# Kernel tuning notes

Hardware: AMD Instinct MI355X
Metric: run time of the kernel (lower is better)

## Reference

```python
import jax, jax.numpy as jnp
import numpy as np

N_NODES = 50000
N_EDGES = 600000
IN_CH, HID1, HID2, OUT_CH = 128, 256, 128, 2


def setup_inputs() -> dict:
    key = jax.random.key(0)
    ks = jax.random.split(key, 8)
    x = jax.random.normal(ks[0], (N_NODES, IN_CH), dtype=jnp.float32)
    edge_index = jax.random.randint(ks[1], (2, N_EDGES), 0, N_NODES, dtype=jnp.int64)
    # Glorot-style init for GCN linear weights
    def glorot(k, fan_in, fan_out):
        s = jnp.sqrt(6.0 / (fan_in + fan_out)).astype(jnp.float32)
        return jax.random.uniform(k, (fan_in, fan_out), jnp.float32, -s, s)
    return {
        "x": x,
        "W1": glorot(ks[2], IN_CH, HID1), "b1": jnp.zeros((HID1,), jnp.float32),
        "W2": glorot(ks[3], HID1, HID2), "b2": jnp.zeros((HID2,), jnp.float32),
        "W3": glorot(ks[4], HID2, OUT_CH), "b3": jnp.zeros((OUT_CH,), jnp.float32),
        "edge_index": edge_index,
    }


def _gcn_graph(edge_index, n_nodes):
    # Add self-loops (GCNConv default) and compute symmetric normalization
    loop = jnp.arange(n_nodes, dtype=edge_index.dtype)
    src = jnp.concatenate([edge_index[0], loop])
    dst = jnp.concatenate([edge_index[1], loop])
    ones = jnp.ones(src.shape[0], dtype=jnp.float32)
    deg = jax.ops.segment_sum(ones, dst, num_segments=n_nodes)
    dinv = jnp.where(deg > 0, jax.lax.rsqrt(deg), 0.0)
    norm = dinv[src] * dinv[dst]  # [E + N]
    return src, dst, norm


def _gcn_layer(h, W, b, src, dst, norm, n_nodes):
    h = h @ W                                   # [N, d_out]
    msg = h[src] * norm[:, None]                # gather + scale  [E+N, d_out]
    agg = jax.ops.segment_sum(msg, dst, num_segments=n_nodes)
    return agg + b


def reference(x, W1, b1, W2, b2, W3, b3, edge_index):
    n = x.shape[0]
    src, dst, norm = _gcn_graph(edge_index, n)
    h = jax.nn.relu(_gcn_layer(x, W1, b1, src, dst, norm, n))
    # dropout p=0.5 is identity in eval mode (training=False)
    h = jax.nn.relu(_gcn_layer(h, W2, b2, src, dst, norm, n))
    h = _gcn_layer(h, W3, b3, src, dst, norm, n)
    return jax.nn.log_softmax(h, axis=1)
```

## Files before the change

kernel.cpp:

```cpp
#include <hip/hip_runtime.h>
#include <hip/hip_bf16.h>
#include <math.h>

#define N_NODES 50000
#define N_EDGES 600000
#define E_TOT   (N_EDGES + N_NODES)
#define M_PAD   50048
#define NODE_STRIDE 32
#define DUMMY_ROWS 65536
#define CSR_CAP (N_NODES * NODE_STRIDE + 2048)

typedef __attribute__((ext_vector_type(8))) short bf16x8;
typedef __attribute__((ext_vector_type(4))) float f32x4;
typedef __attribute__((ext_vector_type(2))) float f32x2;
typedef __attribute__((ext_vector_type(8))) unsigned short u16x8;


__device__ __forceinline__ unsigned short f2bf(float f) {
    unsigned int u = __float_as_uint(f);
    unsigned int r = (u + 0x7fffu + ((u >> 16) & 1u)) >> 16;
    return (unsigned short)r;
}

__device__ __forceinline__ void acc_row(f32x2* acc, uint4 v) {
    acc[0] += (f32x2){__uint_as_float(v.x << 16), __uint_as_float(v.x & 0xffff0000u)};
    acc[1] += (f32x2){__uint_as_float(v.y << 16), __uint_as_float(v.y & 0xffff0000u)};
    acc[2] += (f32x2){__uint_as_float(v.z << 16), __uint_as_float(v.z & 0xffff0000u)};
    acc[3] += (f32x2){__uint_as_float(v.w << 16), __uint_as_float(v.w & 0xffff0000u)};
}

#define GLD_LDS16(g, l) __builtin_amdgcn_global_load_lds( \
    (__attribute__((address_space(1))) void*)(void*)(g), \
    (__attribute__((address_space(3))) void*)(l), 16, 0, 0)


__global__ void prep_kernel(const int* __restrict__ ei, int* __restrict__ cnt,
                            const float* __restrict__ W1, const float* __restrict__ W2,
                            unsigned short* __restrict__ W1t, unsigned short* __restrict__ W2t,
                            unsigned short* __restrict__ csr, unsigned short* __restrict__ xs,
                            unsigned short* __restrict__ t2b, float2* __restrict__ Ts) {
    const int NB_S = (E_TOT + 255) / 256;
    int b = blockIdx.x;
    if (b < NB_S) {
        int e = b * 256 + threadIdx.x;
        if (e >= E_TOT) return;
        int s, d;
        if (e < N_EDGES) { s = ei[e]; d = ei[N_EDGES + e]; }
        else             { s = d = e - N_EDGES; }
        int slot = atomicAdd(&cnt[d], 1);
        if (slot < NODE_STRIDE)
            csr[d * NODE_STRIDE + slot] = (unsigned short)s;
    } else if (b < NB_S + 128) {
        int i = (b - NB_S) * 256 + threadIdx.x;
        int k = i >> 8, n = i & 255;
        W1t[(size_t)n * 128 + k] = f2bf(W1[i]);
    } else if (b < NB_S + 256) {
        int i = (b - NB_S - 128) * 256 + threadIdx.x;
        int k = i >> 7, n = i & 127;
        W2t[(size_t)n * 256 + k] = f2bf(W2[i]);
    } else {
        int t = threadIdx.x;
        if (t < 16)
            *(uint4*)(xs + (size_t)(DUMMY_ROWS - 1) * 128 + t * 8) = make_uint4(0, 0, 0, 0);
        else if (t < 32)
            *(uint4*)(t2b + (size_t)(DUMMY_ROWS - 1) * 128 + (t - 16) * 8) = make_uint4(0, 0, 0, 0);
        else if (t == 32)
            Ts[DUMMY_ROWS - 1] = make_float2(0.f, 0.f);
    }
}


__global__ void scale_kernel(const int* __restrict__ cnt, const float* __restrict__ x,
                             unsigned short* __restrict__ xs, float* __restrict__ dinv) {
    const int NB_C = (N_NODES * 32 + 255) / 256;
    int b = blockIdx.x;
    if (b < NB_C) {
        int i = b * 256 + threadIdx.x;
        if (i >= N_NODES * 32) return;
        float d = rsqrtf((float)cnt[i >> 5]);
        float4 v = *(const float4*)(x + (size_t)i * 4);
        ushort4 o;
        o.x = f2bf(v.x * d); o.y = f2bf(v.y * d); o.z = f2bf(v.z * d); o.w = f2bf(v.w * d);
        *(ushort4*)(xs + (size_t)i * 4) = o;
    } else {
        int i = (b - NB_C) * 256 + threadIdx.x;
        if (i < N_NODES) dinv[i] = rsqrtf((float)cnt[i]);
    }
}


template<bool LAYER2>
__global__ __launch_bounds__(256) void agg_kernel(
    const unsigned short* __restrict__ Hs, const float* __restrict__ dinv,
    const int* __restrict__ cnt, const unsigned short* __restrict__ csr,
    const float* __restrict__ bias, const float* __restrict__ W3,
    unsigned short* __restrict__ outb, float2* __restrict__ Ts) {
    int wave = threadIdx.x >> 6;
    int lane = threadIdx.x & 63;
    int n = blockIdx.x * 4 + wave;
    if (n >= N_NODES) return;
    int quarter = lane >> 4;
    int q = lane & 15;
    f32x2 acc2[4] = {};
    int p0 = n * NODE_STRIDE;
    int pdeg = (cnt[n] + 15) & ~15;
    if (pdeg > NODE_STRIDE) pdeg = NODE_STRIDE;
    int pend = p0 + pdeg;
    int p = p0 + quarter * 4;
    ushort4 s4 = *(const ushort4*)(csr + p);
    while (p < pend) {
        int pn = p + 16;
        ushort4 n4 = *(const ushort4*)(csr + pn);
        uint4 v0 = *(const uint4*)(Hs + (size_t)s4.x * 128 + q * 8);
        uint4 v1 = *(const uint4*)(Hs + (size_t)s4.y * 128 + q * 8);
        uint4 v2 = *(const uint4*)(Hs + (size_t)s4.z * 128 + q * 8);
        uint4 v3 = *(const uint4*)(Hs + (size_t)s4.w * 128 + q * 8);
        acc_row(acc2, v0);
        acc_row(acc2, v1);
        acc_row(acc2, v2);
        acc_row(acc2, v3);
        p = pn; s4 = n4;
    }
    float* acc = (float*)acc2;
    #pragma unroll
    for (int i = 0; i < 8; ++i) {
        acc[i] += __shfl_xor(acc[i], 16);
        acc[i] += __shfl_xor(acc[i], 32);
    }
    float dn = dinv[n];
    if (!LAYER2) {
        if (quarter == 0) {
            u16x8 ov;
            #pragma unroll
            for (int i = 0; i < 8; ++i) ov[i] = f2bf(acc[i] * dn);
            *(u16x8*)(outb + (size_t)n * 128 + q * 8) = ov;
        }
    } else {
        float t0 = 0.f, t1 = 0.f;
        #pragma unroll
        for (int i = 0; i < 8; ++i) {
            int c = q * 8 + i;
            float h = fmaxf(acc[i] * dn + bias[c], 0.f);
            float2 w = ((const float2*)W3)[c];
            t0 += h * w.x; t1 += h * w.y;
        }
        #pragma unroll
        for (int off = 1; off < 16; off <<= 1) {
            t0 += __shfl_xor(t0, off);
            t1 += __shfl_xor(t1, off);
        }
        if (lane == 0) Ts[n] = make_float2(t0 * dn, t1 * dn);
    }
}


__global__ __launch_bounds__(256) void gemm12_kernel(
    const unsigned short* __restrict__ A,
    const unsigned short* __restrict__ W1t,
    const unsigned short* __restrict__ W2t,
    const float* __restrict__ b1,
    const float* __restrict__ rowscale,
    unsigned short* __restrict__ C,
    int M) {
    __shared__ __align__(16) unsigned short h1buf[128 * 256];
    __shared__ __align__(16) unsigned short Bs[64 * 128];
    int tid = threadIdx.x;
    int wave = tid >> 6, lane = tid & 63;
    int m0 = blockIdx.x * 128;
    int mm = lane & 15, kg = lane >> 4;
    int row0 = kg * 4;

    bf16x8 aPre[4][2];
    #pragma unroll
    for (int kt = 0; kt < 4; ++kt)
        #pragma unroll
        for (int i = 0; i < 2; ++i) {
            int m = wave * 32 + i * 16 + mm;
            aPre[kt][i] = *(const bf16x8*)(A + (size_t)(m0 + m) * 128 + kt * 32 + kg * 8);
        }

    int bb[4];
    #pragma unroll
    for (int j = 0; j < 4; ++j) bb[j] = (j * 16 + mm) * 128;
    int h1rd[2];
    #pragma unroll
    for (int i = 0; i < 2; ++i) h1rd[i] = (wave * 32 + i * 16 + mm) * 256;

    #pragma unroll 1
    for (int nt = 0; nt < 4; ++nt) {
        int n0 = nt * 64;
        #pragma unroll
        for (int it = 0; it < 4; ++it) {
            int ci = it * 256 + tid;
            int r = ci >> 4, c8 = (ci & 15) ^ (r & 15);
            const unsigned short* g = W1t + (size_t)(n0 + r) * 128 + c8 * 8;
            unsigned short* l = Bs + (size_t)(it * 256 + (tid & 192)) * 8;
            GLD_LDS16(g, l);
        }
        __syncthreads();
        f32x4 acc[2][4];
        #pragma unroll
        for (int i = 0; i < 2; ++i)
            #pragma unroll
            for (int j = 0; j < 4; ++j)
                acc[i][j] = (f32x4){0.f, 0.f, 0.f, 0.f};
        #pragma unroll
        for (int kt = 0; kt < 4; ++kt) {
            bf16x8 bfr[4];
            #pragma unroll
            for (int j = 0; j < 4; ++j)
                bfr[j] = *(const bf16x8*)(Bs + bb[j] + (((kt * 4 + kg) ^ mm) * 8));
            #pragma unroll
            for (int i = 0; i < 2; ++i)
                #pragma unroll
                for (int j = 0; j < 4; ++j)
                    acc[i][j] = __builtin_amdgcn_mfma_f32_16x16x32_bf16(aPre[kt][i], bfr[j], acc[i][j], 0, 0, 0);
        }
        float bj[4];
        #pragma unroll
        for (int j = 0; j < 4; ++j) bj[j] = b1[n0 + j * 16 + mm];
        #pragma unroll
        for (int i = 0; i < 2; ++i) {
            #pragma unroll
            for (int r = 0; r < 4; ++r) {
                int ml = wave * 32 + i * 16 + row0 + r;
                int rb = ml * 256, rx = ml & 15;
                #pragma unroll
                for (int j = 0; j < 4; ++j) {
                    int c = n0 + j * 16 + mm;
                    int c8 = c >> 3;
                    float v = fmaxf(acc[i][j][r] + bj[j], 0.f);
                    h1buf[rb + ((c8 ^ rx) * 8) + (c & 7)] = f2bf(v);
                }
            }
        }
        __syncthreads();
    }

    #pragma unroll 1
    for (int nh = 0; nh < 2; ++nh) {
        int n0 = nh * 64;
        f32x4 acc[2][4];
        #pragma unroll
        for (int i = 0; i < 2; ++i)
            #pragma unroll
            for (int j = 0; j < 4; ++j)
                acc[i][j] = (f32x4){0.f, 0.f, 0.f, 0.f};
        #pragma unroll 1
        for (int kh = 0; kh < 2; ++kh) {
            #pragma unroll
            for (int it = 0; it < 4; ++it) {
                int ci = it * 256 + tid;
                int r = ci >> 4, c8 = (ci & 15) ^ (r & 15);
                const unsigned short* g = W2t + (size_t)(n0 + r) * 256 + kh * 128 + c8 * 8;
                unsigned short* l = Bs + (size_t)(it * 256 + (tid & 192)) * 8;
                GLD_LDS16(g, l);
            }
            __syncthreads();
            #pragma unroll
            for (int kt = 0; kt < 4; ++kt) {
                bf16x8 af[2], bfr[4];
                int c8h = kh * 16 + kt * 4 + kg;
                #pragma unroll
                for (int i = 0; i < 2; ++i)
                    af[i] = *(const bf16x8*)(h1buf + h1rd[i] + ((c8h ^ mm) * 8));
                #pragma unroll
                for (int j = 0; j < 4; ++j)
                    bfr[j] = *(const bf16x8*)(Bs + bb[j] + (((kt * 4 + kg) ^ mm) * 8));
                #pragma unroll
                for (int i = 0; i < 2; ++i)
                    #pragma unroll
                    for (int j = 0; j < 4; ++j)
                        acc[i][j] = __builtin_amdgcn_mfma_f32_16x16x32_bf16(af[i], bfr[j], acc[i][j], 0, 0, 0);
            }
            __syncthreads();
        }
        #pragma unroll
        for (int i = 0; i < 2; ++i) {
            #pragma unroll
            for (int r = 0; r < 4; ++r) {
                int gm = m0 + wave * 32 + i * 16 + row0 + r;
                float sc = (gm < M) ? rowscale[gm] : 0.f;
                #pragma unroll
                for (int j = 0; j < 4; ++j) {
                    int gn = n0 + j * 16 + mm;
                    C[(size_t)gm * 128 + gn] = f2bf(acc[i][j][r] * sc);
                }
            }
        }
    }
}


__global__ void lsm_kernel(const float2* __restrict__ Ts, const float* __restrict__ dinv,
                           const int* __restrict__ cnt, const unsigned short* __restrict__ csr,
                           const float* __restrict__ b3, float* __restrict__ out) {
    int n = blockIdx.x * 256 + threadIdx.x;
    if (n >= N_NODES) return;
    float a0 = 0.f, a1 = 0.f;
    int p0 = n * NODE_STRIDE;
    int pdeg = (cnt[n] + 3) & ~3;
    if (pdeg > NODE_STRIDE) pdeg = NODE_STRIDE;
    int pend = p0 + pdeg;
    ushort4 s4 = *(const ushort4*)(csr + p0);
    for (int p = p0; p < pend; p += 4) {
        ushort4 n4 = *(const ushort4*)(csr + p + 4);
        float2 u0 = Ts[s4.x], u1 = Ts[s4.y], u2 = Ts[s4.z], u3 = Ts[s4.w];
        a0 += (u0.x + u1.x) + (u2.x + u3.x);
        a1 += (u0.y + u1.y) + (u2.y + u3.y);
        s4 = n4;
    }
    float dn = dinv[n];
    float v0 = a0 * dn + b3[0];
    float v1 = a1 * dn + b3[1];
    float m = fmaxf(v0, v1);
    float lse = m + logf(expf(v0 - m) + expf(v1 - m));
    out[n * 2 + 0] = v0 - lse;
    out[n * 2 + 1] = v1 - lse;
}


extern "C" void kernel_launch(void* const* d_in, const int* in_sizes, int n_in,
                              void* d_out, int out_size, void* d_ws, size_t ws_size,
                              hipStream_t stream) {
    const float* x  = (const float*)d_in[0];
    const float* W1 = (const float*)d_in[1];
    const float* b1 = (const float*)d_in[2];
    const float* W2 = (const float*)d_in[3];
    const float* b2 = (const float*)d_in[4];
    const float* W3 = (const float*)d_in[5];
    const float* b3 = (const float*)d_in[6];
    const int*   ei = (const int*)d_in[7];
    float* out = (float*)d_out;

    char* ws = (char*)d_ws;
    size_t off = 0;
    auto alloc = [&](size_t bytes) -> char* {
        char* p = ws + off;
        off = (off + bytes + 255) & ~(size_t)255;
        return p;
    };
    int*   cnt  = (int*)alloc(N_NODES * 4);
    float* dinv = (float*)alloc(N_NODES * 4);
    unsigned short* csr = (unsigned short*)alloc((size_t)CSR_CAP * 2);
    unsigned short* xs     = (unsigned short*)alloc((size_t)DUMMY_ROWS * 128 * 2);
    unsigned short* W1t    = (unsigned short*)alloc((size_t)256 * 128 * 2);
    unsigned short* W2t    = (unsigned short*)alloc((size_t)128 * 256 * 2);
    unsigned short* aggx_b = (unsigned short*)alloc((size_t)M_PAD * 128 * 2);
    unsigned short* t2b    = (unsigned short*)alloc((size_t)DUMMY_ROWS * 128 * 2);
    float2* Ts = (float2*)alloc((size_t)DUMMY_ROWS * 8);

    hipMemsetAsync(cnt, 0, N_NODES * 4, stream);
    hipMemsetAsync(csr, 0xFF, (size_t)CSR_CAP * 2, stream);

    const int NB_S = (E_TOT + 255) / 256;
    prep_kernel<<<NB_S + 256 + 1, 256, 0, stream>>>(
        ei, cnt, W1, W2, W1t, W2t, csr, xs, t2b, Ts);

    const int NB_C = (N_NODES * 32 + 255) / 256;
    const int NB_D = (N_NODES + 255) / 256;
    scale_kernel<<<NB_C + NB_D, 256, 0, stream>>>(cnt, x, xs, dinv);

    agg_kernel<false><<<(N_NODES + 3) / 4, 256, 0, stream>>>(
        xs, dinv, cnt, csr, nullptr, nullptr, aggx_b, nullptr);
    gemm12_kernel<<<M_PAD / 128, 256, 0, stream>>>(
        aggx_b, W1t, W2t, b1, dinv, t2b, N_NODES);
    agg_kernel<true><<<(N_NODES + 3) / 4, 256, 0, stream>>>(
        t2b, dinv, cnt, csr, b2, W3, nullptr, Ts);

    lsm_kernel<<<(N_NODES + 255) / 256, 256, 0, stream>>>(Ts, dinv, cnt, csr, b3, out);
}
```

Before: 199.4 us.

## Fuse layer-1 aggregation into the GEMM kernel and use 16-lane-per-node gather

The first neighbour aggregation now runs inside the fused GEMM kernel, so each 128-row block gathers its A tile straight into shared memory. This removes the aggregated-feature buffer and one kernel launch. The layer-2 aggregation now gives each node 16 lanes instead of a full wave, which avoids the cross-quarter shuffles and pads the degree to 4 instead of 16. The risk is that the gather inside the GEMM runs on only 391 blocks, one per 128 rows. Each thread group also walks 8 nodes one after another, which could expose gather latency and leave the GPU underused.

```diff
diff --git a/kernel.cpp b/kernel.cpp
--- a/kernel.cpp
+++ b/kernel.cpp
@@ -89,28 +89,207 @@
 }
 
 
-template<bool LAYER2>
-__global__ __launch_bounds__(256) void agg_kernel(
-    const unsigned short* __restrict__ Hs, const float* __restrict__ dinv,
+__global__ __launch_bounds__(256) void gemm12_kernel(
+    const unsigned short* __restrict__ Hs,
+    const float* __restrict__ dinv,
+    const int* __restrict__ cnt,
+    const unsigned short* __restrict__ csr,
+    const unsigned short* __restrict__ W1t,
+    const unsigned short* __restrict__ W2t,
+    const float* __restrict__ b1,
+    unsigned short* __restrict__ C,
+    int M) {
+    __shared__ __align__(16) unsigned short smem[128 * 256 + 64 * 128];
+    unsigned short* Atile = smem;
+    unsigned short* h1buf = smem;
+    unsigned short* Bs    = smem + 128 * 256;
+    int tid = threadIdx.x;
+    int wave = tid >> 6, lane = tid & 63;
+    int m0 = blockIdx.x * 128;
+    int mm = lane & 15, kg = lane >> 4;
+    int row0 = kg * 4;
+
+    {
+        int q = tid & 15;
+        int g = tid >> 4;
+        #pragma unroll 1
+        for (int nn = 0; nn < 8; ++nn) {
+            int r = g * 8 + nn;
+            int n = m0 + r;
+            f32x2 acc2[4] = {};
+            float dn = 0.f;
+            if (n < M) {
+                dn = dinv[n];
+                int p = n * NODE_STRIDE;
+                int pd = (cnt[n] + 3) & ~3;
+                if (pd > NODE_STRIDE) pd = NODE_STRIDE;
+                int pe = p + pd;
+                ushort4 s4 = *(const ushort4*)(csr + p);
+                while (p < pe) {
+                    int pn = p + 4;
+                    ushort4 nx = *(const ushort4*)(csr + pn);
+                    uint4 v0 = *(const uint4*)(Hs + (size_t)s4.x * 128 + q * 8);
+                    uint4 v1 = *(const uint4*)(Hs + (size_t)s4.y * 128 + q * 8);
+                    uint4 v2 = *(const uint4*)(Hs + (size_t)s4.z * 128 + q * 8);
+                    uint4 v3 = *(const uint4*)(Hs + (size_t)s4.w * 128 + q * 8);
+                    acc_row(acc2, v0);
+                    acc_row(acc2, v1);
+                    acc_row(acc2, v2);
+                    acc_row(acc2, v3);
+                    p = pn; s4 = nx;
+                }
+            }
+            float* acc = (float*)acc2;
+            u16x8 ov;
+            #pragma unroll
+            for (int i2 = 0; i2 < 8; ++i2) ov[i2] = f2bf(acc[i2] * dn);
+            *(u16x8*)(Atile + r * 128 + ((q ^ (r & 15)) * 8)) = ov;
+        }
+    }
+    __syncthreads();
+
+    bf16x8 aPre[4][2];
+    #pragma unroll
+    for (int kt = 0; kt < 4; ++kt)
+        #pragma unroll
+        for (int i = 0; i < 2; ++i) {
+            int m = wave * 32 + i * 16 + mm;
+            aPre[kt][i] = *(const bf16x8*)(Atile + m * 128 + (((kt * 4 + kg) ^ (m & 15)) * 8));
+        }
+
+    int bb[4];
+    #pragma unroll
+    for (int j = 0; j < 4; ++j) bb[j] = (j * 16 + mm) * 128;
+    int h1rd[2];
+    #pragma unroll
+    for (int i = 0; i < 2; ++i) h1rd[i] = (wave * 32 + i * 16 + mm) * 256;
+
+    #pragma unroll 1
+    for (int nt = 0; nt < 4; ++nt) {
+        int n0 = nt * 64;
+        #pragma unroll
+        for (int it = 0; it < 4; ++it) {
+            int ci = it * 256 + tid;
+            int r = ci >> 4, c8 = (ci & 15) ^ (r & 15);
+            const unsigned short* g = W1t + (size_t)(n0 + r) * 128 + c8 * 8;
+            unsigned short* l = Bs + (size_t)(it * 256 + (tid & 192)) * 8;
+            GLD_LDS16(g, l);
+        }
+        __syncthreads();
+        f32x4 acc[2][4];
+        #pragma unroll
+        for (int i = 0; i < 2; ++i)
+            #pragma unroll
+            for (int j = 0; j < 4; ++j)
+                acc[i][j] = (f32x4){0.f, 0.f, 0.f, 0.f};
+        #pragma unroll
+        for (int kt = 0; kt < 4; ++kt) {
+            bf16x8 bfr[4];
+            #pragma unroll
+            for (int j = 0; j < 4; ++j)
+                bfr[j] = *(const bf16x8*)(Bs + bb[j] + (((kt * 4 + kg) ^ mm) * 8));
+            #pragma unroll
+            for (int i = 0; i < 2; ++i)
+                #pragma unroll
+                for (int j = 0; j < 4; ++j)
+                    acc[i][j] = __builtin_amdgcn_mfma_f32_16x16x32_bf16(aPre[kt][i], bfr[j], acc[i][j], 0, 0, 0);
+        }
+        float bj[4];
+        #pragma unroll
+        for (int j = 0; j < 4; ++j) bj[j] = b1[n0 + j * 16 + mm];
+        #pragma unroll
+        for (int i = 0; i < 2; ++i) {
+            #pragma unroll
+            for (int r = 0; r < 4; ++r) {
+                int ml = wave * 32 + i * 16 + row0 + r;
+                int rb = ml * 256, rx = ml & 15;
+                #pragma unroll
+                for (int j = 0; j < 4; ++j) {
+                    int c = n0 + j * 16 + mm;
+                    int c8 = c >> 3;
+                    float v = fmaxf(acc[i][j][r] + bj[j], 0.f);
+                    h1buf[rb + ((c8 ^ rx) * 8) + (c & 7)] = f2bf(v);
+                }
+            }
+        }
+        __syncthreads();
+    }
+
+    #pragma unroll 1
+    for (int nh = 0; nh < 2; ++nh) {
+        int n0 = nh * 64;
+        f32x4 acc[2][4];
+        #pragma unroll
+        for (int i = 0; i < 2; ++i)
+            #pragma unroll
+            for (int j = 0; j < 4; ++j)
+                acc[i][j] = (f32x4){0.f, 0.f, 0.f, 0.f};
+        #pragma unroll 1
+        for (int kh = 0; kh < 2; ++kh) {
+            #pragma unroll
+            for (int it = 0; it < 4; ++it) {
+                int ci = it * 256 + tid;
+                int r = ci >> 4, c8 = (ci & 15) ^ (r & 15);
+                const unsigned short* g = W2t + (size_t)(n0 + r) * 256 + kh * 128 + c8 * 8;
+                unsigned short* l = Bs + (size_t)(it * 256 + (tid & 192)) * 8;
+                GLD_LDS16(g, l);
+            }
+            __syncthreads();
+            #pragma unroll
+            for (int kt = 0; kt < 4; ++kt) {
+                bf16x8 af[2], bfr[4];
+                int c8h = kh * 16 + kt * 4 + kg;
+                #pragma unroll
+                for (int i = 0; i < 2; ++i)
+                    af[i] = *(const bf16x8*)(h1buf + h1rd[i] + ((c8h ^ mm) * 8));
+                #pragma unroll
+                for (int j = 0; j < 4; ++j)
+                    bfr[j] = *(const bf16x8*)(Bs + bb[j] + (((kt * 4 + kg) ^ mm) * 8));
+                #pragma unroll
+                for (int i = 0; i < 2; ++i)
+                    #pragma unroll
+                    for (int j = 0; j < 4; ++j)
+                        acc[i][j] = __builtin_amdgcn_mfma_f32_16x16x32_bf16(af[i], bfr[j], acc[i][j], 0, 0, 0);
+            }
+            __syncthreads();
+        }
+        #pragma unroll
+        for (int i = 0; i < 2; ++i) {
+            #pragma unroll
+            for (int r = 0; r < 4; ++r) {
+                int gm = m0 + wave * 32 + i * 16 + row0 + r;
+                float sc = (gm < M) ? dinv[gm] : 0.f;
+                #pragma unroll
+                for (int j = 0; j < 4; ++j) {
+                    int gn = n0 + j * 16 + mm;
+                    C[(size_t)gm * 128 + gn] = f2bf(acc[i][j][r] * sc);
+                }
+            }
+        }
+    }
+}
+
+
+__global__ __launch_bounds__(256) void agg2_kernel(
+    const unsigned short* __restrict__ Hs,
+    const float* __restrict__ dinv,
     const int* __restrict__ cnt, const unsigned short* __restrict__ csr,
-    const float* __restrict__ bias, const float* __restrict__ W3,
-    unsigned short* __restrict__ outb, float2* __restrict__ Ts) {
-    int wave = threadIdx.x >> 6;
-    int lane = threadIdx.x & 63;
-    int n = blockIdx.x * 4 + wave;
+    const float* __restrict__ b2, const float* __restrict__ W3,
+    float2* __restrict__ Ts) {
+    int tid = threadIdx.x;
+    int q = tid & 15;
+    int g = tid >> 4;
+    int n = blockIdx.x * 16 + g;
     if (n >= N_NODES) return;
-    int quarter = lane >> 4;
-    int q = lane & 15;
     f32x2 acc2[4] = {};
-    int p0 = n * NODE_STRIDE;
-    int pdeg = (cnt[n] + 15) & ~15;
-    if (pdeg > NODE_STRIDE) pdeg = NODE_STRIDE;
-    int pend = p0 + pdeg;
-    int p = p0 + quarter * 4;
+    int p = n * NODE_STRIDE;
+    int pd = (cnt[n] + 3) & ~3;
+    if (pd > NODE_STRIDE) pd = NODE_STRIDE;
+    int pe = p + pd;
     ushort4 s4 = *(const ushort4*)(csr + p);
-    while (p < pend) {
-        int pn = p + 16;
-        ushort4 n4 = *(const ushort4*)(csr + pn);
+    while (p < pe) {
+        int pn = p + 4;
+        ushort4 nx = *(const ushort4*)(csr + pn);
         uint4 v0 = *(const uint4*)(Hs + (size_t)s4.x * 128 + q * 8);
         uint4 v1 = *(const uint4*)(Hs + (size_t)s4.y * 128 + q * 8);
         uint4 v2 = *(const uint4*)(Hs + (size_t)s4.z * 128 + q * 8);
@@ -119,176 +298,24 @@
         acc_row(acc2, v1);
         acc_row(acc2, v2);
         acc_row(acc2, v3);
-        p = pn; s4 = n4;
-    }
+        p = pn; s4 = nx;
+    }
+    float dn = dinv[n];
     float* acc = (float*)acc2;
+    float t0 = 0.f, t1 = 0.f;
     #pragma unroll
     for (int i = 0; i < 8; ++i) {
-        acc[i] += __shfl_xor(acc[i], 16);
-        acc[i] += __shfl_xor(acc[i], 32);
-    }
-    float dn = dinv[n];
-    if (!LAYER2) {
-        if (quarter == 0) {
-            u16x8 ov;
-            #pragma unroll
-            for (int i = 0; i < 8; ++i) ov[i] = f2bf(acc[i] * dn);
-            *(u16x8*)(outb + (size_t)n * 128 + q * 8) = ov;
-        }
-    } else {
-        float t0 = 0.f, t1 = 0.f;
-        #pragma unroll
-        for (int i = 0; i < 8; ++i) {
-            int c = q * 8 + i;
-            float h = fmaxf(acc[i] * dn + bias[c], 0.f);
-            float2 w = ((const float2*)W3)[c];
-            t0 += h * w.x; t1 += h * w.y;
-        }
-        #pragma unroll
-        for (int off = 1; off < 16; off <<= 1) {
-            t0 += __shfl_xor(t0, off);
-            t1 += __shfl_xor(t1, off);
-        }
-        if (lane == 0) Ts[n] = make_float2(t0 * dn, t1 * dn);
-    }
-}
-
-
-__global__ __launch_bounds__(256) void gemm12_kernel(
-    const unsigned short* __restrict__ A,
-    const unsigned short* __restrict__ W1t,
-    const unsigned short* __restrict__ W2t,
-    const float* __restrict__ b1,
-    const float* __restrict__ rowscale,
-    unsigned short* __restrict__ C,
-    int M) {
-    __shared__ __align__(16) unsigned short h1buf[128 * 256];
-    __shared__ __align__(16) unsigned short Bs[64 * 128];
-    int tid = threadIdx.x;
-    int wave = tid >> 6, lane = tid & 63;
-    int m0 = blockIdx.x * 128;
-    int mm = lane & 15, kg = lane >> 4;
-    int row0 = kg * 4;
-
-    bf16x8 aPre[4][2];
-    #pragma unroll
-    for (int kt = 0; kt < 4; ++kt)
-        #pragma unroll
-        for (int i = 0; i < 2; ++i) {
-            int m = wave * 32 + i * 16 + mm;
-            aPre[kt][i] = *(const bf16x8*)(A + (size_t)(m0 + m) * 128 + kt * 32 + kg * 8);
-        }
-
-    int bb[4];
-    #pragma unroll
-    for (int j = 0; j < 4; ++j) bb[j] = (j * 16 + mm) * 128;
-    int h1rd[2];
-    #pragma unroll
-    for (int i = 0; i < 2; ++i) h1rd[i] = (wave * 32 + i * 16 + mm) * 256;
-
-    #pragma unroll 1
-    for (int nt = 0; nt < 4; ++nt) {
-        int n0 = nt * 64;
-        #pragma unroll
-        for (int it = 0; it < 4; ++it) {
-            int ci = it * 256 + tid;
-            int r = ci >> 4, c8 = (ci & 15) ^ (r & 15);
-            const unsigned short* g = W1t + (size_t)(n0 + r) * 128 + c8 * 8;
-            unsigned short* l = Bs + (size_t)(it * 256 + (tid & 192)) * 8;
-            GLD_LDS16(g, l);
-        }
-        __syncthreads();
-        f32x4 acc[2][4];
-        #pragma unroll
-        for (int i = 0; i < 2; ++i)
-            #pragma unroll
-            for (int j = 0; j < 4; ++j)
-                acc[i][j] = (f32x4){0.f, 0.f, 0.f, 0.f};
-        #pragma unroll
-        for (int kt = 0; kt < 4; ++kt) {
-            bf16x8 bfr[4];
-            #pragma unroll
-            for (int j = 0; j < 4; ++j)
-                bfr[j] = *(const bf16x8*)(Bs + bb[j] + (((kt * 4 + kg) ^ mm) * 8));
-            #pragma unroll
-            for (int i = 0; i < 2; ++i)
-                #pragma unroll
-                for (int j = 0; j < 4; ++j)
-                    acc[i][j] = __builtin_amdgcn_mfma_f32_16x16x32_bf16(aPre[kt][i], bfr[j], acc[i][j], 0, 0, 0);
-        }
-        float bj[4];
-        #pragma unroll
-        for (int j = 0; j < 4; ++j) bj[j] = b1[n0 + j * 16 + mm];
-        #pragma unroll
-        for (int i = 0; i < 2; ++i) {
-            #pragma unroll
-            for (int r = 0; r < 4; ++r) {
-                int ml = wave * 32 + i * 16 + row0 + r;
-                int rb = ml * 256, rx = ml & 15;
-                #pragma unroll
-                for (int j = 0; j < 4; ++j) {
-                    int c = n0 + j * 16 + mm;
-                    int c8 = c >> 3;
-                    float v = fmaxf(acc[i][j][r] + bj[j], 0.f);
-                    h1buf[rb + ((c8 ^ rx) * 8) + (c & 7)] = f2bf(v);
-                }
-            }
-        }
-        __syncthreads();
-    }
-
-    #pragma unroll 1
-    for (int nh = 0; nh < 2; ++nh) {
-        int n0 = nh * 64;
-        f32x4 acc[2][4];
-        #pragma unroll
-        for (int i = 0; i < 2; ++i)
-            #pragma unroll
-            for (int j = 0; j < 4; ++j)
-                acc[i][j] = (f32x4){0.f, 0.f, 0.f, 0.f};
-        #pragma unroll 1
-        for (int kh = 0; kh < 2; ++kh) {
-            #pragma unroll
-            for (int it = 0; it < 4; ++it) {
-                int ci = it * 256 + tid;
-                int r = ci >> 4, c8 = (ci & 15) ^ (r & 15);
-                const unsigned short* g = W2t + (size_t)(n0 + r) * 256 + kh * 128 + c8 * 8;
-                unsigned short* l = Bs + (size_t)(it * 256 + (tid & 192)) * 8;
-                GLD_LDS16(g, l);
-            }
-            __syncthreads();
-            #pragma unroll
-            for (int kt = 0; kt < 4; ++kt) {
-                bf16x8 af[2], bfr[4];
-                int c8h = kh * 16 + kt * 4 + kg;
-                #pragma unroll
-                for (int i = 0; i < 2; ++i)
-                    af[i] = *(const bf16x8*)(h1buf + h1rd[i] + ((c8h ^ mm) * 8));
-                #pragma unroll
-                for (int j = 0; j < 4; ++j)
-                    bfr[j] = *(const bf16x8*)(Bs + bb[j] + (((kt * 4 + kg) ^ mm) * 8));
-                #pragma unroll
-                for (int i = 0; i < 2; ++i)
-                    #pragma unroll
-                    for (int j = 0; j < 4; ++j)
-                        acc[i][j] = __builtin_amdgcn_mfma_f32_16x16x32_bf16(af[i], bfr[j], acc[i][j], 0, 0, 0);
-            }
-            __syncthreads();
-        }
-        #pragma unroll
-        for (int i = 0; i < 2; ++i) {
-            #pragma unroll
-            for (int r = 0; r < 4; ++r) {
-                int gm = m0 + wave * 32 + i * 16 + row0 + r;
-                float sc = (gm < M) ? rowscale[gm] : 0.f;
-                #pragma unroll
-                for (int j = 0; j < 4; ++j) {
-                    int gn = n0 + j * 16 + mm;
-                    C[(size_t)gm * 128 + gn] = f2bf(acc[i][j][r] * sc);
-                }
-            }
-        }
-    }
+        int c = q * 8 + i;
+        float h = fmaxf(acc[i] * dn + b2[c], 0.f);
+        float2 w = ((const float2*)W3)[c];
+        t0 += h * w.x; t1 += h * w.y;
+    }
+    #pragma unroll
+    for (int off = 1; off < 16; off <<= 1) {
+        t0 += __shfl_xor(t0, off);
+        t1 += __shfl_xor(t1, off);
+    }
+    if (q == 0) Ts[n] = make_float2(t0 * dn, t1 * dn);
 }
 
 
@@ -346,7 +373,6 @@
     unsigned short* xs     = (unsigned short*)alloc((size_t)DUMMY_ROWS * 128 * 2);
     unsigned short* W1t    = (unsigned short*)alloc((size_t)256 * 128 * 2);
     unsigned short* W2t    = (unsigned short*)alloc((size_t)128 * 256 * 2);
-    unsigned short* aggx_b = (unsigned short*)alloc((size_t)M_PAD * 128 * 2);
     unsigned short* t2b    = (unsigned short*)alloc((size_t)DUMMY_ROWS * 128 * 2);
     float2* Ts = (float2*)alloc((size_t)DUMMY_ROWS * 8);
 
@@ -361,12 +387,10 @@
     const int NB_D = (N_NODES + 255) / 256;
     scale_kernel<<<NB_C + NB_D, 256, 0, stream>>>(cnt, x, xs, dinv);
 
-    agg_kernel<false><<<(N_NODES + 3) / 4, 256, 0, stream>>>(
-        xs, dinv, cnt, csr, nullptr, nullptr, aggx_b, nullptr);
     gemm12_kernel<<<M_PAD / 128, 256, 0, stream>>>(
-        aggx_b, W1t, W2t, b1, dinv, t2b, N_NODES);
-    agg_kernel<true><<<(N_NODES + 3) / 4, 256, 0, stream>>>(
-        t2b, dinv, cnt, csr, b2, W3, nullptr, Ts);
+        xs, dinv, cnt, csr, W1t, W2t, b1, t2b, N_NODES);
+    agg2_kernel<<<(N_NODES + 15) / 16, 256, 0, stream>>>(
+        t2b, dinv, cnt, csr, b2, W3, Ts);
 
     lsm_kernel<<<(N_NODES + 255) / 256, 256, 0, stream>>>(Ts, dinv, cnt, csr, b3, out);
 }
```

Measured after the change: 199.6 us. Within noise of the previous version (+0.1%).
